# Kernel optimization log

Hardware: AMD Instinct MI355X
Metric: run time of the kernel (lower is better)

## Reference

```python
import jax, jax.numpy as jnp
import numpy as np
from jax import lax

V, E, H, T, S = 100000, 256, 512, 9, 4096
HH = H // 2
START, STOP = 7, 8
NEG = -10000.0


def setup_inputs() -> dict:
    key = jax.random.key(0)
    ks = jax.random.split(key, 16)
    def n(k, shape, scale=0.1):
        return jax.random.normal(k, shape, jnp.float32) * scale
    sentence = jax.random.randint(ks[0], (S,), 0, V)
    embed = n(ks[1], (V, E), 1.0)
    w_ih_f = n(ks[2], (4 * HH, E)); w_hh_f = n(ks[3], (4 * HH, HH))
    b_ih_f = n(ks[4], (4 * HH,));   b_hh_f = n(ks[5], (4 * HH,))
    w_ih_b = n(ks[6], (4 * HH, E)); w_hh_b = n(ks[7], (4 * HH, HH))
    b_ih_b = n(ks[8], (4 * HH,));   b_hh_b = n(ks[9], (4 * HH,))
    h0 = n(ks[10], (2, HH), 1.0)  # init_hidden: randn (2,1,HH), batch squeezed
    c0 = n(ks[11], (2, HH), 1.0)
    W_out = n(ks[12], (T, H)); b_out = n(ks[13], (T,))
    transitions = jax.random.normal(ks[14], (T, T), jnp.float32)
    transitions = transitions.at[START, :].set(NEG).at[:, STOP].set(NEG)
    return dict(sentence=sentence, embed=embed,
                w_ih_f=w_ih_f, w_hh_f=w_hh_f, b_ih_f=b_ih_f, b_hh_f=b_hh_f,
                w_ih_b=w_ih_b, w_hh_b=w_hh_b, b_ih_b=b_ih_b, b_hh_b=b_hh_b,
                h0=h0, c0=c0, W_out=W_out, b_out=b_out, transitions=transitions)


def _lstm_dir(x_gates, h0, c0, w_hh):
    # x_gates: [S, 4*HH] = x @ w_ih.T + b_ih + b_hh (precomputed input part)
    def step(carry, xg):
        h, c = carry
        g = xg + h @ w_hh.T
        i, f, gg, o = jnp.split(g, 4)  # torch gate order: i, f, g, o
        i = jax.nn.sigmoid(i); f = jax.nn.sigmoid(f)
        gg = jnp.tanh(gg);     o = jax.nn.sigmoid(o)
        c = f * c + i * gg
        h = o * jnp.tanh(c)
        return (h, c), h
    _, hs = lax.scan(step, (h0, c0), x_gates)
    return hs  # [S, HH]


def reference(sentence, embed, w_ih_f, w_hh_f, b_ih_f, b_hh_f,
              w_ih_b, w_hh_b, b_ih_b, b_hh_b, h0, c0, W_out, b_out, transitions):
    x = embed[sentence]  # [S, E]
    # bidirectional LSTM, batch=1
    hf = _lstm_dir(x @ w_ih_f.T + b_ih_f + b_hh_f, h0[0], c0[0], w_hh_f)
    hb = _lstm_dir((x @ w_ih_b.T + b_ih_b + b_hh_b)[::-1], h0[1], c0[1], w_hh_b)[::-1]
    lstm_out = jnp.concatenate([hf, hb], axis=-1)          # [S, H]
    frames = lstm_out @ W_out.T + b_out                     # [S, T] emission scores

    # Viterbi-style decode (faithful: alpha updated by logsumexp, backpointers by argmax)
    alpha0 = jnp.full((T,), NEG, jnp.float32).at[START].set(0.0)
    def vstep(alpha, frame):
        smat = alpha[:, None] + frame[None, :] + transitions  # [T, T]
        bp = jnp.argmax(smat, axis=0)
        return jax.nn.logsumexp(smat, axis=0), bp
    alpha, bps = lax.scan(vstep, alpha0, frames)            # bps: [S, T]

    final = alpha + transitions[:, STOP]                     # [T]
    best = jnp.argmax(final)
    score = jax.nn.logsumexp(final)

    # backtrack over bps[1:] in reverse
    def bstep(tag, bp):
        nt = bp[tag]
        return nt, nt
    _, path_rev = lax.scan(bstep, best, bps[1:][::-1])
    tag_seq = jnp.concatenate([path_rev[::-1], best[None]])  # [S]
    return score, tag_seq
```

## Files before the change

kernel.cpp:

```cpp
#include <hip/hip_runtime.h>
#include <hip/hip_bf16.h>

#define SEQ   4096
#define EMB   256
#define HHID  256
#define G4    1024
#define NT    9
#define TSTART 7
#define TSTOP  8
#define NEGV  (-10000.0f)
#define POISON 0xAAAAAAAAu

#define WS_XG_F   0u
#define WS_XG_B   16777216u
#define WS_HF     33554432u
#define WS_HB     37748736u
#define WS_FRAMES 41943040u

__global__ __launch_bounds__(256) void xgate_kernel(
    const int* __restrict__ sentence, const float* __restrict__ embed,
    const float* __restrict__ w_ih_f, const float* __restrict__ b_ih_f,
    const float* __restrict__ b_hh_f,
    const float* __restrict__ w_ih_b, const float* __restrict__ b_ih_b,
    const float* __restrict__ b_hh_b,
    float* __restrict__ xg_f, float* __restrict__ xg_b)
{
    const int st  = blockIdx.x;
    const int dir = blockIdx.y;
    const float* w  = dir ? w_ih_b : w_ih_f;
    const float* bi = dir ? b_ih_b : b_ih_f;
    const float* bh = dir ? b_hh_b : b_hh_f;
    float* xg = dir ? xg_b : xg_f;
    const int t = threadIdx.x;

    __shared__ float x_t[EMB][16];
    for (int sl = 0; sl < 16; ++sl) {
        int s   = st * 16 + sl;
        int tok = sentence[s];
        x_t[t][sl] = embed[(size_t)tok * EMB + t];
    }
    __syncthreads();

    float acc[4][16];
    #pragma unroll
    for (int q = 0; q < 4; ++q)
        #pragma unroll
        for (int sl = 0; sl < 16; ++sl) acc[q][sl] = 0.f;

    #pragma unroll 4
    for (int e = 0; e < EMB; ++e) {
        float w0 = w[(size_t)(t        ) * EMB + e];
        float w1 = w[(size_t)(t + 256  ) * EMB + e];
        float w2 = w[(size_t)(t + 512  ) * EMB + e];
        float w3 = w[(size_t)(t + 768  ) * EMB + e];
        #pragma unroll
        for (int sl = 0; sl < 16; ++sl) {
            float xv = x_t[e][sl];
            acc[0][sl] += w0 * xv;
            acc[1][sl] += w1 * xv;
            acc[2][sl] += w2 * xv;
            acc[3][sl] += w3 * xv;
        }
    }

    #pragma unroll
    for (int q = 0; q < 4; ++q) {
        int g = t + 256 * q;
        float bb = bi[g] + bh[g];
        for (int sl = 0; sl < 16; ++sl) {
            xg[(size_t)(st * 16 + sl) * G4 + g] = acc[q][sl] + bb;
        }
    }
}

__global__ __launch_bounds__(256, 1) void lstm_kernel(
    const float* __restrict__ xg_f, const float* __restrict__ xg_b,
    const float* __restrict__ w_hh_f, const float* __restrict__ w_hh_b,
    const float* __restrict__ h0, const float* __restrict__ c0,
    float* __restrict__ hf, float* __restrict__ hb)
{
    const int bx    = blockIdx.x;
    const int dir   = bx >> 3;
    const int slice = bx & 7;
    const int t     = threadIdx.x;
    const int cb    = t & 7;
    const int rb    = t >> 3;
    const int unit  = slice * 32 + rb;

    const float* xg   = dir ? xg_b  : xg_f;
    const float* w_hh = dir ? w_hh_b : w_hh_f;
    float* hout = dir ? hb : hf;

    __shared__ float buf[2][HHID];

    float wa[128];
    #pragma unroll
    for (int q = 0; q < 4; ++q) {
        #pragma unroll
        for (int j = 0; j < 32; ++j) {
            float tmp = w_hh[(size_t)(q * HHID + unit) * HHID + cb * 32 + j];
            asm volatile("v_accvgpr_write_b32 %0, %1"
                         : "=a"(wa[q * 32 + j]) : "v"(tmp));
        }
    }

    float c_reg = 0.f;
    if (cb == 0) c_reg = c0[dir * HHID + unit];

    const bool own = (t >= slice * 32) && (t < slice * 32 + 32);

    for (int n = 0; n < SEQ; ++n) {
        const int s = dir ? (SEQ - 1 - n) : n;

        float xg0 = 0.f, xg1 = 0.f, xg2 = 0.f, xg3 = 0.f;
        if (cb == 0) {
            const float* xb = xg + (size_t)s * G4 + unit;
            xg0 = xb[0];
            xg1 = xb[HHID];
            xg2 = xb[2 * HHID];
            xg3 = xb[3 * HHID];
        }

        if (n == 0) {
            buf[0][t] = h0[dir * HHID + t];
        } else if (!own) {
            const int sp = dir ? (s + 1) : (s - 1);
            const unsigned int* src =
                (const unsigned int*)(hout + (size_t)sp * HHID) + t;
            unsigned v;
            do {
                v = __hip_atomic_load(src, __ATOMIC_RELAXED,
                                      __HIP_MEMORY_SCOPE_AGENT);
            } while (v == POISON);
            buf[n & 1][t] = __uint_as_float(v);
        }
        __syncthreads();

        float a0 = 0.f, a1 = 0.f, a2 = 0.f, a3 = 0.f;
        const float4* h4 = (const float4*)(&buf[n & 1][cb * 32]);
        #pragma unroll
        for (int j4 = 0; j4 < 8; ++j4) {
            float4 hv = h4[j4];
            #pragma unroll
            for (int k = 0; k < 4; ++k) {
                float hk = (k == 0) ? hv.x : (k == 1) ? hv.y
                         : (k == 2) ? hv.z : hv.w;
                float w0, w1, w2, w3;
                asm volatile("v_accvgpr_read_b32 %0, %1"
                             : "=v"(w0) : "a"(wa[0 * 32 + j4 * 4 + k]));
                asm volatile("v_accvgpr_read_b32 %0, %1"
                             : "=v"(w1) : "a"(wa[1 * 32 + j4 * 4 + k]));
                asm volatile("v_accvgpr_read_b32 %0, %1"
                             : "=v"(w2) : "a"(wa[2 * 32 + j4 * 4 + k]));
                asm volatile("v_accvgpr_read_b32 %0, %1"
                             : "=v"(w3) : "a"(wa[3 * 32 + j4 * 4 + k]));
                a0 += w0 * hk;
                a1 += w1 * hk;
                a2 += w2 * hk;
                a3 += w3 * hk;
            }
        }

        #pragma unroll
        for (int m = 1; m <= 4; m <<= 1) {
            a0 += __shfl_xor(a0, m);
            a1 += __shfl_xor(a1, m);
            a2 += __shfl_xor(a2, m);
            a3 += __shfl_xor(a3, m);
        }

        if (cb == 0) {
            float gi = a0 + xg0;
            float gf = a1 + xg1;
            float gg = a2 + xg2;
            float go = a3 + xg3;
            float iv = 1.f / (1.f + __expf(-gi));
            float fv = 1.f / (1.f + __expf(-gf));
            float gv = 1.f - 2.f / (__expf(2.f * gg) + 1.f);
            float ov = 1.f / (1.f + __expf(-go));
            float c  = fv * c_reg + iv * gv;
            c_reg = c;
            float h  = ov * (1.f - 2.f / (__expf(2.f * c) + 1.f));
            unsigned int* dst =
                (unsigned int*)(hout + (size_t)s * HHID) + unit;
            __hip_atomic_store(dst, __float_as_uint(h), __ATOMIC_RELAXED,
                               __HIP_MEMORY_SCOPE_AGENT);
            buf[(n + 1) & 1][unit] = h;
        }
    }
}

__global__ __launch_bounds__(256) void frames_kernel(
    const float* __restrict__ hf, const float* __restrict__ hb,
    const float* __restrict__ W_out, const float* __restrict__ b_out,
    float* __restrict__ frames)
{
    int o = blockIdx.x * 256 + threadIdx.x;
    if (o >= SEQ * NT) return;
    int s = o / NT;
    int j = o - s * NT;
    const float4* a0 = (const float4*)(hf + (size_t)s * HHID);
    const float4* a1 = (const float4*)(hb + (size_t)s * HHID);
    const float4* w0 = (const float4*)(W_out + (size_t)j * 512);
    const float4* w1 = w0 + 64;
    float acc = 0.f;
    #pragma unroll 8
    for (int i = 0; i < 64; ++i) {
        float4 a = a0[i], b = w0[i];
        acc += a.x * b.x + a.y * b.y + a.z * b.z + a.w * b.w;
        float4 c = a1[i], d = w1[i];
        acc += c.x * d.x + c.y * d.y + c.z * d.z + c.w * d.w;
    }
    frames[o] = acc + b_out[j];
}

__global__ __launch_bounds__(64) void crf_kernel(
    const float* __restrict__ frames, const float* __restrict__ trans,
    float* __restrict__ dout)
{
    __shared__ float fr[512 * NT];
    __shared__ unsigned char bpl[SEQ * NT];
    const int t = threadIdx.x;
    const int tc = (t < NT) ? t : 0;

    float trow[NT];
    #pragma unroll
    for (int i = 0; i < NT; ++i) trow[i] = 0.f;
    if (t < NT) {
        #pragma unroll
        for (int i = 0; i < NT; ++i) trow[i] = trans[i * NT + t];
    }
    float alpha = (t == TSTART) ? 0.f : NEGV;

    for (int chunk = 0; chunk < 8; ++chunk) {
        for (int idx = t; idx < 512 * NT; idx += 64)
            fr[idx] = frames[chunk * 512 * NT + idx];
        __syncthreads();

        for (int sl = 0; sl < 512; ++sl) {
            const int s = chunk * 512 + sl;
            float v[NT];
            #pragma unroll
            for (int i = 0; i < NT; ++i)
                v[i] = __shfl(alpha, i) + trow[i];
            float mx = v[0];
            int   am = 0;
            #pragma unroll
            for (int i = 1; i < NT; ++i)
                if (v[i] > mx) { mx = v[i]; am = i; }
            float sum = 0.f;
            #pragma unroll
            for (int i = 0; i < NT; ++i) sum += __expf(v[i] - mx);
            float anew = fr[sl * NT + tc] + mx + __logf(sum);
            if (t < NT) {
                bpl[s * NT + t] = (unsigned char)am;
                alpha = anew;
            }
        }
        __syncthreads();
    }

    float fin = NEGV;
    if (t < NT) fin = alpha + trans[t * NT + TSTOP];
    float f[NT];
    #pragma unroll
    for (int j = 0; j < NT; ++j) f[j] = __shfl(fin, j);

    if (t == 0) {
        float mx = f[0];
        int best = 0;
        #pragma unroll
        for (int j = 1; j < NT; ++j)
            if (f[j] > mx) { mx = f[j]; best = j; }
        float sum = 0.f;
        #pragma unroll
        for (int j = 0; j < NT; ++j) sum += __expf(f[j] - mx);
        dout[0] = mx + __logf(sum);

        int cur = best;
        dout[1 + SEQ - 1] = (float)cur;
        for (int s = SEQ - 2; s >= 0; --s) {
            cur = bpl[(s + 1) * NT + cur];
            dout[1 + s] = (float)cur;
        }
    }
}

extern "C" void kernel_launch(void* const* d_in, const int* in_sizes, int n_in,
                              void* d_out, int out_size, void* d_ws, size_t ws_size,
                              hipStream_t stream)
{
    const int*   sentence = (const int*)  d_in[0];
    const float* embed    = (const float*)d_in[1];
    const float* w_ih_f   = (const float*)d_in[2];
    const float* w_hh_f   = (const float*)d_in[3];
    const float* b_ih_f   = (const float*)d_in[4];
    const float* b_hh_f   = (const float*)d_in[5];
    const float* w_ih_b   = (const float*)d_in[6];
    const float* w_hh_b   = (const float*)d_in[7];
    const float* b_ih_b   = (const float*)d_in[8];
    const float* b_hh_b   = (const float*)d_in[9];
    const float* h0       = (const float*)d_in[10];
    const float* c0       = (const float*)d_in[11];
    const float* W_out    = (const float*)d_in[12];
    const float* b_out    = (const float*)d_in[13];
    const float* trans    = (const float*)d_in[14];

    float* out = (float*)d_out;
    char*  ws  = (char*)d_ws;

    float* xg_f   = (float*)(ws + WS_XG_F);
    float* xg_b   = (float*)(ws + WS_XG_B);
    float* hf     = (float*)(ws + WS_HF);
    float* hb     = (float*)(ws + WS_HB);
    float* frames = (float*)(ws + WS_FRAMES);

    hipMemsetAsync(hf, 0xAA, 2u * SEQ * HHID * sizeof(float), stream);

    xgate_kernel<<<dim3(256, 2), 256, 0, stream>>>(
        sentence, embed, w_ih_f, b_ih_f, b_hh_f, w_ih_b, b_ih_b, b_hh_b,
        xg_f, xg_b);

    lstm_kernel<<<16, 256, 0, stream>>>(
        xg_f, xg_b, w_hh_f, w_hh_b, h0, c0, hf, hb);

    frames_kernel<<<(SEQ * NT + 255) / 256, 256, 0, stream>>>(
        hf, hb, W_out, b_out, frames);

    crf_kernel<<<1, 64, 0, stream>>>(frames, trans, out);
}
```

Before: 9.920 ms.

## Pin LSTM recurrence blocks to one XCC and prefetch input gates ahead

Launches many blocks and lets only the first 16 that land on XCC 0 claim roles through an atomic counter, so all cooperating recurrence blocks share one L2 and cross-block hidden-state exchange stays out of slower cross-die paths. Input-gate values are now prefetched three steps ahead into a register ring buffer, and the poll and store of hidden states use raw loads and stores with cache-policy bits instead of agent-scope atomics. This adds a claim counter memset, extra idle blocks that exit immediately, and relies on scheduling and cache-coherence assumptions that could deadlock or read stale data if wrong.

```diff
diff --git a/kernel.cpp b/kernel.cpp
--- a/kernel.cpp
+++ b/kernel.cpp
@@ -16,6 +16,7 @@
 #define WS_HF     33554432u
 #define WS_HB     37748736u
 #define WS_FRAMES 41943040u
+#define WS_CLAIM  42090496u
 
 __global__ __launch_bounds__(256) void xgate_kernel(
     const int* __restrict__ sentence, const float* __restrict__ embed,
@@ -77,11 +78,26 @@
     const float* __restrict__ xg_f, const float* __restrict__ xg_b,
     const float* __restrict__ w_hh_f, const float* __restrict__ w_hh_b,
     const float* __restrict__ h0, const float* __restrict__ c0,
-    float* __restrict__ hf, float* __restrict__ hb)
-{
-    const int bx    = blockIdx.x;
-    const int dir   = bx >> 3;
-    const int slice = bx & 7;
+    float* __restrict__ hf, float* __restrict__ hb,
+    unsigned int* __restrict__ claim)
+{
+    unsigned int xcc;
+    asm volatile("s_getreg_b32 %0, hwreg(HW_REG_XCC_ID)" : "=s"(xcc));
+    __shared__ int role_s;
+    if (threadIdx.x == 0) {
+        int role = -1;
+        if (xcc == 0u) {
+            unsigned int slot = atomicAdd(claim, 1u);
+            if (slot < 16u) role = (int)slot;
+        }
+        role_s = role;
+    }
+    __syncthreads();
+    const int role = role_s;
+    if (role < 0) return;
+
+    const int dir   = role >> 3;
+    const int slice = role & 7;
     const int t     = threadIdx.x;
     const int cb    = t & 7;
     const int rb    = t >> 3;
@@ -109,83 +125,121 @@
 
     const bool own = (t >= slice * 32) && (t < slice * 32 + 32);
 
-    for (int n = 0; n < SEQ; ++n) {
-        const int s = dir ? (SEQ - 1 - n) : n;
-
-        float xg0 = 0.f, xg1 = 0.f, xg2 = 0.f, xg3 = 0.f;
-        if (cb == 0) {
-            const float* xb = xg + (size_t)s * G4 + unit;
-            xg0 = xb[0];
-            xg1 = xb[HHID];
-            xg2 = xb[2 * HHID];
-            xg3 = xb[3 * HHID];
-        }
-
-        if (n == 0) {
-            buf[0][t] = h0[dir * HHID + t];
-        } else if (!own) {
-            const int sp = dir ? (s + 1) : (s - 1);
-            const unsigned int* src =
-                (const unsigned int*)(hout + (size_t)sp * HHID) + t;
-            unsigned v;
-            do {
-                v = __hip_atomic_load(src, __ATOMIC_RELAXED,
-                                      __HIP_MEMORY_SCOPE_AGENT);
-            } while (v == POISON);
-            buf[n & 1][t] = __uint_as_float(v);
-        }
-        __syncthreads();
-
-        float a0 = 0.f, a1 = 0.f, a2 = 0.f, a3 = 0.f;
-        const float4* h4 = (const float4*)(&buf[n & 1][cb * 32]);
-        #pragma unroll
-        for (int j4 = 0; j4 < 8; ++j4) {
-            float4 hv = h4[j4];
-            #pragma unroll
-            for (int k = 0; k < 4; ++k) {
-                float hk = (k == 0) ? hv.x : (k == 1) ? hv.y
-                         : (k == 2) ? hv.z : hv.w;
-                float w0, w1, w2, w3;
-                asm volatile("v_accvgpr_read_b32 %0, %1"
-                             : "=v"(w0) : "a"(wa[0 * 32 + j4 * 4 + k]));
-                asm volatile("v_accvgpr_read_b32 %0, %1"
-                             : "=v"(w1) : "a"(wa[1 * 32 + j4 * 4 + k]));
-                asm volatile("v_accvgpr_read_b32 %0, %1"
-                             : "=v"(w2) : "a"(wa[2 * 32 + j4 * 4 + k]));
-                asm volatile("v_accvgpr_read_b32 %0, %1"
-                             : "=v"(w3) : "a"(wa[3 * 32 + j4 * 4 + k]));
-                a0 += w0 * hk;
-                a1 += w1 * hk;
-                a2 += w2 * hk;
-                a3 += w3 * hk;
-            }
-        }
-
-        #pragma unroll
-        for (int m = 1; m <= 4; m <<= 1) {
-            a0 += __shfl_xor(a0, m);
-            a1 += __shfl_xor(a1, m);
-            a2 += __shfl_xor(a2, m);
-            a3 += __shfl_xor(a3, m);
-        }
-
-        if (cb == 0) {
-            float gi = a0 + xg0;
-            float gf = a1 + xg1;
-            float gg = a2 + xg2;
-            float go = a3 + xg3;
-            float iv = 1.f / (1.f + __expf(-gi));
-            float fv = 1.f / (1.f + __expf(-gf));
-            float gv = 1.f - 2.f / (__expf(2.f * gg) + 1.f);
-            float ov = 1.f / (1.f + __expf(-go));
-            float c  = fv * c_reg + iv * gv;
-            c_reg = c;
-            float h  = ov * (1.f - 2.f / (__expf(2.f * c) + 1.f));
-            unsigned int* dst =
-                (unsigned int*)(hout + (size_t)s * HHID) + unit;
-            __hip_atomic_store(dst, __float_as_uint(h), __ATOMIC_RELAXED,
-                               __HIP_MEMORY_SCOPE_AGENT);
-            buf[(n + 1) & 1][unit] = h;
+    float xgb[4][4];
+    #pragma unroll
+    for (int b = 0; b < 4; ++b)
+        #pragma unroll
+        for (int j = 0; j < 4; ++j) xgb[b][j] = 0.f;
+    if (cb == 0) {
+        #pragma unroll
+        for (int m = 0; m < 3; ++m) {
+            const int sm = dir ? (SEQ - 1 - m) : m;
+            const float* xb = xg + (size_t)sm * G4 + unit;
+            xgb[m][0] = xb[0];
+            xgb[m][1] = xb[HHID];
+            xgb[m][2] = xb[2 * HHID];
+            xgb[m][3] = xb[3 * HHID];
+        }
+    }
+
+    for (int nb = 0; nb < SEQ; nb += 4) {
+        #pragma unroll
+        for (int u = 0; u < 4; ++u) {
+            const int n = nb + u;
+            const int s = dir ? (SEQ - 1 - n) : n;
+
+            if (n == 0) {
+                buf[0][t] = h0[dir * HHID + t];
+            } else if (!own) {
+                const int sp = dir ? (s + 1) : (s - 1);
+                const unsigned int* src =
+                    (const unsigned int*)(hout + (size_t)sp * HHID) + t;
+                unsigned int v;
+                int k = 0;
+                while (true) {
+                    if ((k & 7) == 7) {
+                        v = __hip_atomic_load(src, __ATOMIC_RELAXED,
+                                              __HIP_MEMORY_SCOPE_AGENT);
+                    } else {
+                        asm volatile(
+                            "global_load_dword %0, %1, off sc0\n\t"
+                            "s_waitcnt vmcnt(0)"
+                            : "=v"(v) : "v"(src) : "memory");
+                    }
+                    ++k;
+                    if (v != POISON) break;
+                }
+                buf[u & 1][t] = __uint_as_float(v);
+            }
+
+            {
+                const int m = n + 3;
+                if (cb == 0 && m < SEQ) {
+                    const int sm = dir ? (SEQ - 1 - m) : m;
+                    const float* xb = xg + (size_t)sm * G4 + unit;
+                    float* d = xgb[(u + 3) & 3];
+                    d[0] = xb[0];
+                    d[1] = xb[HHID];
+                    d[2] = xb[2 * HHID];
+                    d[3] = xb[3 * HHID];
+                }
+            }
+            __syncthreads();
+
+            float a0 = 0.f, a1 = 0.f, a2 = 0.f, a3 = 0.f;
+            const float4* h4 = (const float4*)(&buf[u & 1][cb * 32]);
+            #pragma unroll
+            for (int j4 = 0; j4 < 8; ++j4) {
+                float4 hv = h4[j4];
+                #pragma unroll
+                for (int k = 0; k < 4; ++k) {
+                    float hk = (k == 0) ? hv.x : (k == 1) ? hv.y
+                             : (k == 2) ? hv.z : hv.w;
+                    float w0, w1, w2, w3;
+                    asm volatile("v_accvgpr_read_b32 %0, %1"
+                                 : "=v"(w0) : "a"(wa[0 * 32 + j4 * 4 + k]));
+                    asm volatile("v_accvgpr_read_b32 %0, %1"
+                                 : "=v"(w1) : "a"(wa[1 * 32 + j4 * 4 + k]));
+                    asm volatile("v_accvgpr_read_b32 %0, %1"
+                                 : "=v"(w2) : "a"(wa[2 * 32 + j4 * 4 + k]));
+                    asm volatile("v_accvgpr_read_b32 %0, %1"
+                                 : "=v"(w3) : "a"(wa[3 * 32 + j4 * 4 + k]));
+                    a0 += w0 * hk;
+                    a1 += w1 * hk;
+                    a2 += w2 * hk;
+                    a3 += w3 * hk;
+                }
+            }
+
+            #pragma unroll
+            for (int m = 1; m <= 4; m <<= 1) {
+                a0 += __shfl_xor(a0, m);
+                a1 += __shfl_xor(a1, m);
+                a2 += __shfl_xor(a2, m);
+                a3 += __shfl_xor(a3, m);
+            }
+
+            if (cb == 0) {
+                float gi = a0 + xgb[u][0];
+                float gf = a1 + xgb[u][1];
+                float gg = a2 + xgb[u][2];
+                float go = a3 + xgb[u][3];
+                float iv = 1.f / (1.f + __expf(-gi));
+                float fv = 1.f / (1.f + __expf(-gf));
+                float gv = 1.f - 2.f / (__expf(2.f * gg) + 1.f);
+                float ov = 1.f / (1.f + __expf(-go));
+                float c  = fv * c_reg + iv * gv;
+                c_reg = c;
+                float h  = ov * (1.f - 2.f / (__expf(2.f * c) + 1.f));
+                unsigned int hbits = __float_as_uint(h);
+                unsigned int* dst =
+                    (unsigned int*)(hout + (size_t)s * HHID) + unit;
+                asm volatile(
+                    "global_store_dword %0, %1, off sc0\n\t"
+                    "global_store_dword %0, %1, off sc1"
+                    :: "v"(dst), "v"(hbits) : "memory");
+                buf[(u + 1) & 1][unit] = h;
+            }
         }
     }
 }
@@ -314,15 +368,17 @@
     float* hf     = (float*)(ws + WS_HF);
     float* hb     = (float*)(ws + WS_HB);
     float* frames = (float*)(ws + WS_FRAMES);
+    unsigned int* claim = (unsigned int*)(ws + WS_CLAIM);
 
     hipMemsetAsync(hf, 0xAA, 2u * SEQ * HHID * sizeof(float), stream);
+    hipMemsetAsync(claim, 0, 256, stream);
 
     xgate_kernel<<<dim3(256, 2), 256, 0, stream>>>(
         sentence, embed, w_ih_f, b_ih_f, b_hh_f, w_ih_b, b_ih_b, b_hh_b,
         xg_f, xg_b);
 
-    lstm_kernel<<<16, 256, 0, stream>>>(
-        xg_f, xg_b, w_hh_f, w_hh_b, h0, c0, hf, hb);
+    lstm_kernel<<<2048, 256, 0, stream>>>(
+        xg_f, xg_b, w_hh_f, w_hh_b, h0, c0, hf, hb, claim);
 
     frames_kernel<<<(SEQ * NT + 255) / 256, 256, 0, stream>>>(
         hf, hb, W_out, b_out, frames);
```

New measurement: 15.78 ms. 59.1% more time.
